# Optimization experiments

Measured on AMD Instinct MI355X. Metric: run time of the kernel, lower is better.

## Reference

```python
import jax, jax.numpy as jnp
import numpy as np

N_NODES = 100000
N_EDGES = 640000
IN_D = 128
OUT_D = 128


def setup_inputs() -> dict:
    key = jax.random.key(0)
    k_x, k_ei, k_ws, k_wn = jax.random.split(key, 4)
    scale = 1.0 / np.sqrt(IN_D)
    return {
        "x": jax.random.normal(k_x, (N_NODES, IN_D), dtype=jnp.float32),
        "ei": jax.random.randint(k_ei, (2, N_EDGES), 0, N_NODES, dtype=jnp.int64),
        "Ws": jax.random.normal(k_ws, (IN_D, OUT_D), dtype=jnp.float32) * scale,
        "bs": jnp.zeros((OUT_D,), dtype=jnp.float32),
        "Wn": jax.random.normal(k_wn, (IN_D, OUT_D), dtype=jnp.float32) * scale,
        "bn": jnp.zeros((OUT_D,), dtype=jnp.float32),
    }


def reference(x, ei, Ws, bs, Wn, bn):
    # x: [N, in_d], ei: [2, E]
    src, dst = ei[0], ei[1]
    n = x.shape[0]
    # scatter-sum of gathered source features onto destinations
    agg = jax.ops.segment_sum(x[src], dst, num_segments=n)  # [N, in_d]
    # in-degree per destination node
    deg = jax.ops.segment_sum(jnp.ones(src.shape[0], dtype=x.dtype), dst, num_segments=n)  # [N]
    agg = agg / jnp.maximum(deg, 1.0)[:, None]
    # dual linear + relu (dropout is identity in eval)
    return jax.nn.relu(x @ Ws + bs + agg @ Wn + bn)
```

## Files before the change

### kernel.cpp

```cpp
#include <hip/hip_runtime.h>
#include <hip/hip_bf16.h>

#define D 128

typedef __attribute__((ext_vector_type(8))) short short8v;
typedef __attribute__((ext_vector_type(4))) float f32x4;

__device__ __forceinline__ short f2bf(float f) {
    union { float f; unsigned u; } v;
    v.f = f;
    unsigned u = v.u;
    unsigned r = (u + 0x7FFFu + ((u >> 16) & 1u)) >> 16;
    return (short)r;
}

__device__ __forceinline__ float bf2f(unsigned u16) {
    union { unsigned u; float f; } v;
    v.u = u16 << 16;
    return v.f;
}

__device__ __forceinline__ unsigned pkbf2(float lo, float hi) {
    __hip_bfloat162 h = __float22bfloat162_rn(make_float2(lo, hi));
    union { __hip_bfloat162 h; unsigned u; } v;
    v.h = h;
    return v.u;
}

__global__ __launch_bounds__(256) void prep_kernel(const int* __restrict__ dst,
                                                   int* __restrict__ counts, int nE,
                                                   const float* __restrict__ Ws,
                                                   const float* __restrict__ Wn,
                                                   short* __restrict__ WT2,
                                                   const float* __restrict__ x,
                                                   unsigned short* __restrict__ xb,
                                                   int nElem) {
    const int nbE = (nE + 255) >> 8;
    const int b = blockIdx.x;
    if (b < nbE) {
        int e = b * 256 + threadIdx.x;
        if (e < nE) atomicAdd(&counts[dst[e]], 1);
    } else if (b < nbE + 128) {
        int idx = (b - nbE) * 256 + threadIdx.x;
        int nn = idx >> 8;
        int k = idx & 255;
        float v = (k < D) ? Ws[k * D + nn] : Wn[(k - D) * D + nn];
        WT2[idx] = f2bf(v);
    } else {
        int idx = (b - nbE - 128) * 256 + threadIdx.x;
        int base = idx * 8;
        if (base < nElem) {
            float4 lo = *reinterpret_cast<const float4*>(x + base);
            float4 hi = *reinterpret_cast<const float4*>(x + base + 4);
            union { short8v s8; unsigned u[4]; } p;
            p.u[0] = pkbf2(lo.x, lo.y);
            p.u[1] = pkbf2(lo.z, lo.w);
            p.u[2] = pkbf2(hi.x, hi.y);
            p.u[3] = pkbf2(hi.z, hi.w);
            *reinterpret_cast<short8v*>(xb + base) = p.s8;
        }
    }
}

__global__ __launch_bounds__(256) void scan_partial_kernel(const int* __restrict__ counts,
                                                           int* __restrict__ bsums, int n) {
    __shared__ int wsum[4];
    const int t = threadIdx.x;
    const int i0 = blockIdx.x * 1024 + t * 4;
    int s = 0;
#pragma unroll
    for (int j = 0; j < 4; ++j) s += (i0 + j < n) ? counts[i0 + j] : 0;
#pragma unroll
    for (int off = 32; off > 0; off >>= 1) s += __shfl_down(s, off, 64);
    if ((t & 63) == 0) wsum[t >> 6] = s;
    __syncthreads();
    if (t == 0) bsums[blockIdx.x] = wsum[0] + wsum[1] + wsum[2] + wsum[3];
}

__global__ __launch_bounds__(128) void scan_bsums_kernel(const int* __restrict__ bsums,
                                                         int* __restrict__ ebsums,
                                                         int* __restrict__ rowptr_n,
                                                         int nb) {
    __shared__ int sh[128];
    const int t = threadIdx.x;
    int v = (t < nb) ? bsums[t] : 0;
    sh[t] = v;
    __syncthreads();
    for (int off = 1; off < 128; off <<= 1) {
        int u = (t >= off) ? sh[t - off] : 0;
        __syncthreads();
        sh[t] += u;
        __syncthreads();
    }
    if (t < nb) ebsums[t] = sh[t] - v;
    if (t == 127) *rowptr_n = sh[127];
}

__global__ __launch_bounds__(256) void scan_final_kernel(int* __restrict__ counts,
                                                         const int* __restrict__ ebsums,
                                                         int* __restrict__ rowptr, int n) {
    __shared__ int sh[256];
    const int t = threadIdx.x;
    const int i0 = blockIdx.x * 1024 + t * 4;
    int c[4];
    int s = 0;
#pragma unroll
    for (int j = 0; j < 4; ++j) {
        c[j] = (i0 + j < n) ? counts[i0 + j] : 0;
        s += c[j];
    }
    sh[t] = s;
    __syncthreads();
    for (int off = 1; off < 256; off <<= 1) {
        int u = (t >= off) ? sh[t - off] : 0;
        __syncthreads();
        sh[t] += u;
        __syncthreads();
    }
    int run = ebsums[blockIdx.x] + sh[t] - s;
#pragma unroll
    for (int j = 0; j < 4; ++j) {
        int i = i0 + j;
        if (i < n) {
            rowptr[i] = run;
            counts[i] = run;
            run += c[j];
        }
    }
}

__global__ __launch_bounds__(256) void fill_kernel(const int* __restrict__ src,
                                                   const int* __restrict__ dst,
                                                   int* __restrict__ cursor,
                                                   int* __restrict__ csr, int nE) {
    int e = blockIdx.x * 256 + threadIdx.x;
    if (e < nE) {
        int pos = atomicAdd(&cursor[dst[e]], 1);
        csr[pos] = src[e];
    }
}

__global__ __launch_bounds__(256) void gather_kernel(const int* __restrict__ rowptr,
                                                     const int* __restrict__ csr,
                                                     const unsigned short* __restrict__ xb,
                                                     unsigned* __restrict__ aggOut,
                                                     int n) {
    const int wave = threadIdx.x >> 6;
    const int lane = threadIdx.x & 63;
    const int d = blockIdx.x * 4 + wave;
    if (d >= n) return;

    const int beg = rowptr[d];
    const int end = rowptr[d + 1];
    float ax = 0.f, ay = 0.f;

    int i = beg;
    for (; i + 3 < end; i += 4) {
        int s0 = csr[i], s1 = csr[i + 1], s2 = csr[i + 2], s3 = csr[i + 3];
        unsigned v0 = *reinterpret_cast<const unsigned*>(xb + (size_t)s0 * D + lane * 2);
        unsigned v1 = *reinterpret_cast<const unsigned*>(xb + (size_t)s1 * D + lane * 2);
        unsigned v2 = *reinterpret_cast<const unsigned*>(xb + (size_t)s2 * D + lane * 2);
        unsigned v3 = *reinterpret_cast<const unsigned*>(xb + (size_t)s3 * D + lane * 2);
        ax += (bf2f(v0 & 0xffffu) + bf2f(v1 & 0xffffu)) +
              (bf2f(v2 & 0xffffu) + bf2f(v3 & 0xffffu));
        ay += (bf2f(v0 >> 16) + bf2f(v1 >> 16)) + (bf2f(v2 >> 16) + bf2f(v3 >> 16));
    }
    for (; i < end; ++i) {
        unsigned v0 = *reinterpret_cast<const unsigned*>(xb + (size_t)csr[i] * D + lane * 2);
        ax += bf2f(v0 & 0xffffu);
        ay += bf2f(v0 >> 16);
    }

    const float inv = 1.0f / fmaxf((float)(end - beg), 1.0f);
    aggOut[(size_t)d * D + lane] = pkbf2(ax * inv, ay * inv);
}

__global__ __launch_bounds__(256) void gemm_kernel(const unsigned short* __restrict__ xb,
                                                   const short* __restrict__ WT2,
                                                   const float* __restrict__ bs,
                                                   const float* __restrict__ bn,
                                                   const unsigned* __restrict__ aggIn,
                                                   float* __restrict__ out,
                                                   int n, int nStrips) {
    const int wave = threadIdx.x >> 6;
    const int lane = threadIdx.x & 63;
    const int lrow = lane & 15;
    const int q = lane >> 4;
    const int ko = q * 8;

    short8v b[2][8];
#pragma unroll
    for (int j = 0; j < 2; ++j) {
        const short* __restrict__ wp = WT2 + (size_t)((wave * 2 + j) * 16 + lrow) * 256 + ko;
#pragma unroll
        for (int ks = 0; ks < 8; ++ks)
            b[j][ks] = *reinterpret_cast<const short8v*>(wp + ks * 32);
    }
    float bias[2];
#pragma unroll
    for (int j = 0; j < 2; ++j) {
        int c = (wave * 2 + j) * 16 + lrow;
        bias[j] = bs[c] + bn[c];
    }

    for (int strip = blockIdx.x; strip < nStrips; strip += gridDim.x) {
        const int m0 = strip * 16;

        short8v a[8];
        const unsigned short* __restrict__ xr = xb + (size_t)(m0 + lrow) * D + ko;
        const unsigned* __restrict__ ar = aggIn + (size_t)(m0 + lrow) * D;
#pragma unroll
        for (int ks = 0; ks < 4; ++ks) {
            a[ks] = *reinterpret_cast<const short8v*>(xr + ks * 32);
            union { uint4 u4; short8v s8; } cv;
            cv.u4 = *reinterpret_cast<const uint4*>(ar + q * 4 + ks * 16);
            a[4 + ks] = cv.s8;
        }

        __syncthreads();

        f32x4 acc[2];
        acc[0] = (f32x4){0.f, 0.f, 0.f, 0.f};
        acc[1] = (f32x4){0.f, 0.f, 0.f, 0.f};
#pragma unroll
        for (int j = 0; j < 2; ++j)
#pragma unroll
            for (int ks = 0; ks < 8; ++ks)
                acc[j] = __builtin_amdgcn_mfma_f32_16x16x32_bf16(a[ks], b[j][ks], acc[j], 0, 0, 0);

        const int r0 = m0 + q * 4;
#pragma unroll
        for (int j = 0; j < 2; ++j) {
            const int c = (wave * 2 + j) * 16 + lrow;
#pragma unroll
            for (int rg = 0; rg < 4; ++rg) {
                int r = r0 + rg;
                if (r < n) out[(size_t)r * D + c] = fmaxf(acc[j][rg] + bias[j], 0.f);
            }
        }
    }
}

extern "C" void kernel_launch(void* const* d_in, const int* in_sizes, int n_in,
                              void* d_out, int out_size, void* d_ws, size_t ws_size,
                              hipStream_t stream) {
    const float* x  = (const float*)d_in[0];
    const int*   ei = (const int*)d_in[1];
    const float* Ws = (const float*)d_in[2];
    const float* bs = (const float*)d_in[3];
    const float* Wn = (const float*)d_in[4];
    const float* bn = (const float*)d_in[5];
    float* out = (float*)d_out;

    const int n  = in_sizes[0] / D;
    const int nE = in_sizes[1] / 2;
    const int* src = ei;
    const int* dst = ei + nE;
    const int nb = (n + 1023) / 1024;
    const int nElem = n * D;

    unsigned short* xb = (unsigned short*)d_ws;
    short* WT2   = (short*)(xb + (size_t)nElem);
    int*   counts = (int*)(WT2 + (size_t)D * 256);
    int*   rowptr = counts + n;
    int*   csr    = rowptr + n + 1;
    int*   bsums  = csr + nE;
    int*   ebsums = bsums + 128;

    const int nbE = (nE + 255) / 256;
    const int nXb = (nElem / 8 + 255) / 256;

    hipMemsetAsync(counts, 0, (size_t)n * sizeof(int), stream);
    prep_kernel<<<nbE + 128 + nXb, 256, 0, stream>>>(dst, counts, nE, Ws, Wn, WT2, x, xb, nElem);
    scan_partial_kernel<<<nb, 256, 0, stream>>>(counts, bsums, n);
    scan_bsums_kernel<<<1, 128, 0, stream>>>(bsums, ebsums, rowptr + n, nb);
    scan_final_kernel<<<nb, 256, 0, stream>>>(counts, ebsums, rowptr, n);
    fill_kernel<<<(nE + 255) / 256, 256, 0, stream>>>(src, dst, counts, csr, nE);

    gather_kernel<<<(n + 3) / 4, 256, 0, stream>>>(rowptr, csr, xb, (unsigned*)out, n);

    const int nStrips = (n + 15) / 16;
    const int gGrid = nStrips < 2048 ? nStrips : 2048;
    gemm_kernel<<<gGrid, 256, 0, stream>>>(xb, WT2, bs, bn, (const unsigned*)out, out, n, nStrips);
}
```

Measured before the change: 170.5 us.

## Fuse scan into single grid-synced kernel, gather two nodes per wave, vectorize GEMM stores

Replaces the three-kernel prefix scan with one kernel that publishes block sums, spins on a global counter until all blocks arrive, then reduces the sums itself. This removes two launches but relies on every block being co-resident. The gather kernel now has each wave interleave the edge lists of two destination nodes, to expose more independent loads. The GEMM swaps its MFMA operands so each lane holds four consecutive output columns, enabling float4 bias loads and float4 stores; the row-bound check on stores is dropped.

```diff
diff --git a/kernel.cpp b/kernel.cpp
--- a/kernel.cpp
+++ b/kernel.cpp
@@ -62,46 +62,16 @@
     }
 }
 
-__global__ __launch_bounds__(256) void scan_partial_kernel(const int* __restrict__ counts,
-                                                           int* __restrict__ bsums, int n) {
-    __shared__ int wsum[4];
+__global__ __launch_bounds__(256) void scan_fused_kernel(int* __restrict__ counts,
+                                                         int* __restrict__ bsums,
+                                                         int* __restrict__ done,
+                                                         int* __restrict__ rowptr,
+                                                         int n, int nb) {
+    __shared__ int sh[256];
+    __shared__ int s_base, s_total;
+    const int b = blockIdx.x;
     const int t = threadIdx.x;
-    const int i0 = blockIdx.x * 1024 + t * 4;
-    int s = 0;
-#pragma unroll
-    for (int j = 0; j < 4; ++j) s += (i0 + j < n) ? counts[i0 + j] : 0;
-#pragma unroll
-    for (int off = 32; off > 0; off >>= 1) s += __shfl_down(s, off, 64);
-    if ((t & 63) == 0) wsum[t >> 6] = s;
-    __syncthreads();
-    if (t == 0) bsums[blockIdx.x] = wsum[0] + wsum[1] + wsum[2] + wsum[3];
-}
-
-__global__ __launch_bounds__(128) void scan_bsums_kernel(const int* __restrict__ bsums,
-                                                         int* __restrict__ ebsums,
-                                                         int* __restrict__ rowptr_n,
-                                                         int nb) {
-    __shared__ int sh[128];
-    const int t = threadIdx.x;
-    int v = (t < nb) ? bsums[t] : 0;
-    sh[t] = v;
-    __syncthreads();
-    for (int off = 1; off < 128; off <<= 1) {
-        int u = (t >= off) ? sh[t - off] : 0;
-        __syncthreads();
-        sh[t] += u;
-        __syncthreads();
-    }
-    if (t < nb) ebsums[t] = sh[t] - v;
-    if (t == 127) *rowptr_n = sh[127];
-}
-
-__global__ __launch_bounds__(256) void scan_final_kernel(int* __restrict__ counts,
-                                                         const int* __restrict__ ebsums,
-                                                         int* __restrict__ rowptr, int n) {
-    __shared__ int sh[256];
-    const int t = threadIdx.x;
-    const int i0 = blockIdx.x * 1024 + t * 4;
+    const int i0 = b * 1024 + t * 4;
     int c[4];
     int s = 0;
 #pragma unroll
@@ -117,7 +87,31 @@
         sh[t] += u;
         __syncthreads();
     }
-    int run = ebsums[blockIdx.x] + sh[t] - s;
+    const int blockAgg = sh[255];
+    if (t == 0) {
+        bsums[b] = blockAgg;
+        __threadfence();
+        atomicAdd(done, 1);
+        while (atomicAdd(done, 0) < nb) { }
+    }
+    __syncthreads();
+    int xv = (t < nb) ? atomicAdd(&bsums[t], 0) : 0;
+    int vb = (t < b) ? xv : 0;
+#pragma unroll
+    for (int off = 32; off > 0; off >>= 1) {
+        vb += __shfl_down(vb, off, 64);
+        xv += __shfl_down(xv, off, 64);
+    }
+    if (t == 0) { s_base = vb; s_total = xv; }
+    else if (t == 64 && nb > 64) { atomicAdd(&s_base, 0); }
+    __syncthreads();
+    if (t == 64) {
+        atomicAdd(&s_base, vb);
+        atomicAdd(&s_total, xv);
+    }
+    __syncthreads();
+    const int base = s_base;
+    int run = base + sh[t] - s;
 #pragma unroll
     for (int j = 0; j < 4; ++j) {
         int i = i0 + j;
@@ -127,6 +121,7 @@
             run += c[j];
         }
     }
+    if (b == nb - 1 && t == 0) rowptr[n] = s_total;
 }
 
 __global__ __launch_bounds__(256) void fill_kernel(const int* __restrict__ src,
@@ -147,32 +142,66 @@
                                                      int n) {
     const int wave = threadIdx.x >> 6;
     const int lane = threadIdx.x & 63;
-    const int d = blockIdx.x * 4 + wave;
-    if (d >= n) return;
-
-    const int beg = rowptr[d];
-    const int end = rowptr[d + 1];
-    float ax = 0.f, ay = 0.f;
-
-    int i = beg;
-    for (; i + 3 < end; i += 4) {
-        int s0 = csr[i], s1 = csr[i + 1], s2 = csr[i + 2], s3 = csr[i + 3];
-        unsigned v0 = *reinterpret_cast<const unsigned*>(xb + (size_t)s0 * D + lane * 2);
-        unsigned v1 = *reinterpret_cast<const unsigned*>(xb + (size_t)s1 * D + lane * 2);
-        unsigned v2 = *reinterpret_cast<const unsigned*>(xb + (size_t)s2 * D + lane * 2);
-        unsigned v3 = *reinterpret_cast<const unsigned*>(xb + (size_t)s3 * D + lane * 2);
-        ax += (bf2f(v0 & 0xffffu) + bf2f(v1 & 0xffffu)) +
-              (bf2f(v2 & 0xffffu) + bf2f(v3 & 0xffffu));
-        ay += (bf2f(v0 >> 16) + bf2f(v1 >> 16)) + (bf2f(v2 >> 16) + bf2f(v3 >> 16));
-    }
-    for (; i < end; ++i) {
-        unsigned v0 = *reinterpret_cast<const unsigned*>(xb + (size_t)csr[i] * D + lane * 2);
-        ax += bf2f(v0 & 0xffffu);
-        ay += bf2f(v0 >> 16);
-    }
-
-    const float inv = 1.0f / fmaxf((float)(end - beg), 1.0f);
-    aggOut[(size_t)d * D + lane] = pkbf2(ax * inv, ay * inv);
+    const int d0 = blockIdx.x * 8 + wave * 2;
+    if (d0 >= n) return;
+    const bool has1 = (d0 + 1) < n;
+
+    int iA = rowptr[d0];
+    const int endA = rowptr[d0 + 1];
+    int iB = has1 ? endA : 0;
+    const int endB = has1 ? rowptr[d0 + 2] : 0;
+    const int ofs = lane * 2;
+
+    float ax0 = 0.f, ay0 = 0.f, ax1 = 0.f, ay1 = 0.f;
+
+    while (iA + 2 <= endA && iB + 2 <= endB) {
+        int a0 = csr[iA], a1 = csr[iA + 1], b0 = csr[iB], b1 = csr[iB + 1];
+        unsigned v0 = *reinterpret_cast<const unsigned*>(xb + (size_t)a0 * D + ofs);
+        unsigned v1 = *reinterpret_cast<const unsigned*>(xb + (size_t)a1 * D + ofs);
+        unsigned w0 = *reinterpret_cast<const unsigned*>(xb + (size_t)b0 * D + ofs);
+        unsigned w1 = *reinterpret_cast<const unsigned*>(xb + (size_t)b1 * D + ofs);
+        ax0 += bf2f(v0 & 0xffffu) + bf2f(v1 & 0xffffu);
+        ay0 += bf2f(v0 >> 16) + bf2f(v1 >> 16);
+        ax1 += bf2f(w0 & 0xffffu) + bf2f(w1 & 0xffffu);
+        ay1 += bf2f(w0 >> 16) + bf2f(w1 >> 16);
+        iA += 2;
+        iB += 2;
+    }
+    while (iA + 2 <= endA) {
+        int a0 = csr[iA], a1 = csr[iA + 1];
+        unsigned v0 = *reinterpret_cast<const unsigned*>(xb + (size_t)a0 * D + ofs);
+        unsigned v1 = *reinterpret_cast<const unsigned*>(xb + (size_t)a1 * D + ofs);
+        ax0 += bf2f(v0 & 0xffffu) + bf2f(v1 & 0xffffu);
+        ay0 += bf2f(v0 >> 16) + bf2f(v1 >> 16);
+        iA += 2;
+    }
+    while (iB + 2 <= endB) {
+        int b0 = csr[iB], b1 = csr[iB + 1];
+        unsigned w0 = *reinterpret_cast<const unsigned*>(xb + (size_t)b0 * D + ofs);
+        unsigned w1 = *reinterpret_cast<const unsigned*>(xb + (size_t)b1 * D + ofs);
+        ax1 += bf2f(w0 & 0xffffu) + bf2f(w1 & 0xffffu);
+        ay1 += bf2f(w0 >> 16) + bf2f(w1 >> 16);
+        iB += 2;
+    }
+    if (iA < endA) {
+        unsigned v0 = *reinterpret_cast<const unsigned*>(xb + (size_t)csr[iA] * D + ofs);
+        ax0 += bf2f(v0 & 0xffffu);
+        ay0 += bf2f(v0 >> 16);
+    }
+    if (iB < endB) {
+        unsigned w0 = *reinterpret_cast<const unsigned*>(xb + (size_t)csr[iB] * D + ofs);
+        ax1 += bf2f(w0 & 0xffffu);
+        ay1 += bf2f(w0 >> 16);
+    }
+
+    const int degA = endA - iA + (iA - rowptr[d0]);
+    const float invA = 1.0f / fmaxf((float)(endA - rowptr[d0]), 1.0f);
+    aggOut[(size_t)d0 * D + lane] = pkbf2(ax0 * invA, ay0 * invA);
+    (void)degA;
+    if (has1) {
+        const float invB = 1.0f / fmaxf((float)(endB - endA), 1.0f);
+        aggOut[(size_t)(d0 + 1) * D + lane] = pkbf2(ax1 * invB, ay1 * invB);
+    }
 }
 
 __global__ __launch_bounds__(256) void gemm_kernel(const unsigned short* __restrict__ xb,
@@ -196,11 +225,13 @@
         for (int ks = 0; ks < 8; ++ks)
             b[j][ks] = *reinterpret_cast<const short8v*>(wp + ks * 32);
     }
-    float bias[2];
+    float4 bias[2];
 #pragma unroll
     for (int j = 0; j < 2; ++j) {
-        int c = (wave * 2 + j) * 16 + lrow;
-        bias[j] = bs[c] + bn[c];
+        const int cb = (wave * 2 + j) * 16 + q * 4;
+        float4 v1 = *reinterpret_cast<const float4*>(bs + cb);
+        float4 v2 = *reinterpret_cast<const float4*>(bn + cb);
+        bias[j] = make_float4(v1.x + v2.x, v1.y + v2.y, v1.z + v2.z, v1.w + v2.w);
     }
 
     for (int strip = blockIdx.x; strip < nStrips; strip += gridDim.x) {
@@ -226,17 +257,18 @@
         for (int j = 0; j < 2; ++j)
 #pragma unroll
             for (int ks = 0; ks < 8; ++ks)
-                acc[j] = __builtin_amdgcn_mfma_f32_16x16x32_bf16(a[ks], b[j][ks], acc[j], 0, 0, 0);
-
-        const int r0 = m0 + q * 4;
+                acc[j] = __builtin_amdgcn_mfma_f32_16x16x32_bf16(b[j][ks], a[ks], acc[j], 0, 0, 0);
+
+        const size_t rb = (size_t)(m0 + lrow) * D;
 #pragma unroll
         for (int j = 0; j < 2; ++j) {
-            const int c = (wave * 2 + j) * 16 + lrow;
-#pragma unroll
-            for (int rg = 0; rg < 4; ++rg) {
-                int r = r0 + rg;
-                if (r < n) out[(size_t)r * D + c] = fmaxf(acc[j][rg] + bias[j], 0.f);
-            }
+            const int cb = (wave * 2 + j) * 16 + q * 4;
+            float4 o;
+            o.x = fmaxf(acc[j][0] + bias[j].x, 0.f);
+            o.y = fmaxf(acc[j][1] + bias[j].y, 0.f);
+            o.z = fmaxf(acc[j][2] + bias[j].z, 0.f);
+            o.w = fmaxf(acc[j][3] + bias[j].w, 0.f);
+            *reinterpret_cast<float4*>(out + rb + cb) = o;
         }
     }
 }
@@ -262,22 +294,20 @@
     unsigned short* xb = (unsigned short*)d_ws;
     short* WT2   = (short*)(xb + (size_t)nElem);
     int*   counts = (int*)(WT2 + (size_t)D * 256);
-    int*   rowptr = counts + n;
+    int*   bsums  = counts + n;
+    int*   done   = bsums + 128;
+    int*   rowptr = done + 1;
     int*   csr    = rowptr + n + 1;
-    int*   bsums  = csr + nE;
-    int*   ebsums = bsums + 128;
 
     const int nbE = (nE + 255) / 256;
     const int nXb = (nElem / 8 + 255) / 256;
 
-    hipMemsetAsync(counts, 0, (size_t)n * sizeof(int), stream);
+    hipMemsetAsync(counts, 0, (size_t)(n + 129) * sizeof(int), stream);
     prep_kernel<<<nbE + 128 + nXb, 256, 0, stream>>>(dst, counts, nE, Ws, Wn, WT2, x, xb, nElem);
-    scan_partial_kernel<<<nb, 256, 0, stream>>>(counts, bsums, n);
-    scan_bsums_kernel<<<1, 128, 0, stream>>>(bsums, ebsums, rowptr + n, nb);
-    scan_final_kernel<<<nb, 256, 0, stream>>>(counts, ebsums, rowptr, n);
+    scan_fused_kernel<<<nb, 256, 0, stream>>>(counts, bsums, done, rowptr, n, nb);
     fill_kernel<<<(nE + 255) / 256, 256, 0, stream>>>(src, dst, counts, csr, nE);
 
-    gather_kernel<<<(n + 3) / 4, 256, 0, stream>>>(rowptr, csr, xb, (unsigned*)out, n);
+    gather_kernel<<<(n + 7) / 8, 256, 0, stream>>>(rowptr, csr, xb, (unsigned*)out, n);
 
     const int nStrips = (n + 15) / 16;
     const int gGrid = nStrips < 2048 ? nStrips : 2048;
```

Result: faster. 165.6 us (-2.9%).
